# Optimization experiments

Hardware: AMD Instinct MI355X
Metric: run time of the kernel (lower is better)

The kernel has to match this reference:

```python
import jax, jax.numpy as jnp
import numpy as np

N = 50000      # num nodes
E = 800000     # num edges (before self loops)
DIN = 128      # input_dim
HID = 32       # hidden_dim per head
HEADS = 4
DOUT = 128     # output_dim
NEG_SLOPE = 0.2
EPS = 1e-5


def setup_inputs() -> dict:
    key = jax.random.key(0)
    ks = jax.random.split(key, 16)
    s = 0.05
    return {
        "x": jax.random.normal(ks[0], (N, DIN), dtype=jnp.float32),
        "edge_index": jax.random.randint(ks[1], (2, E), 0, N, dtype=jnp.int64),
        # GAT layer 1 (heads=4, concat=True)
        "W1": jax.random.normal(ks[2], (DIN, HEADS * HID), dtype=jnp.float32) * s,
        "att_src1": jax.random.normal(ks[3], (HEADS, HID), dtype=jnp.float32) * s,
        "att_dst1": jax.random.normal(ks[4], (HEADS, HID), dtype=jnp.float32) * s,
        "b1": jnp.zeros((HEADS * HID,), dtype=jnp.float32),
        # GAT layer 2 (heads=1, concat=False)
        "W2": jax.random.normal(ks[5], (HEADS * HID, DOUT), dtype=jnp.float32) * s,
        "att_src2": jax.random.normal(ks[6], (1, DOUT), dtype=jnp.float32) * s,
        "att_dst2": jax.random.normal(ks[7], (1, DOUT), dtype=jnp.float32) * s,
        "b2": jnp.zeros((DOUT,), dtype=jnp.float32),
        # LayerNorms
        "g1": jnp.ones((HEADS * HID,), dtype=jnp.float32),
        "be1": jnp.zeros((HEADS * HID,), dtype=jnp.float32),
        "g2": jnp.ones((DOUT,), dtype=jnp.float32),
        "be2": jnp.zeros((DOUT,), dtype=jnp.float32),
    }


def gat_conv(x, src, dst, W, a_src, a_dst, n_nodes):
    # x: [N, Fin]; W: [Fin, H*C]; a_src/a_dst: [H, C]
    H, C = a_src.shape
    h = (x @ W).reshape(-1, H, C)                       # [N, H, C]
    es = jnp.einsum("nhc,hc->nh", h, a_src)             # [N, H]
    ed = jnp.einsum("nhc,hc->nh", h, a_dst)             # [N, H]
    e = jax.nn.leaky_relu(es[src] + ed[dst], NEG_SLOPE)  # [E, H]
    # segment softmax over incoming edges of each dst node
    m = jax.ops.segment_max(e, dst, num_segments=n_nodes)
    a = jnp.exp(e - jax.lax.stop_gradient(m)[dst])
    den = jax.ops.segment_sum(a, dst, num_segments=n_nodes)
    alpha = a / den[dst]                                 # [E, H]
    out = jax.ops.segment_sum(alpha[:, :, None] * h[src], dst,
                              num_segments=n_nodes)      # [N, H, C]
    return out


def layer_norm(x, g, b):
    mu = jnp.mean(x, axis=-1, keepdims=True)
    var = jnp.mean((x - mu) ** 2, axis=-1, keepdims=True)
    return (x - mu) * jax.lax.rsqrt(var + EPS) * g + b


def reference(x, edge_index, W1, att_src1, att_dst1, b1,
              W2, att_src2, att_dst2, b2, g1, be1, g2, be2):
    n = x.shape[0]
    loop = jnp.arange(n, dtype=edge_index.dtype)
    src = jnp.concatenate([edge_index[0], loop])  # PyG add_self_loops=True
    dst = jnp.concatenate([edge_index[1], loop])

    h = gat_conv(x, src, dst, W1, att_src1, att_dst1, n)   # [N, 4, 32]
    h = h.reshape(n, -1) + b1                              # concat=True
    h = jax.nn.relu(layer_norm(h, g1, be1))                # dropout = id (eval)

    o = gat_conv(h, src, dst, W2, att_src2, att_dst2, n)   # [N, 1, DOUT]
    o = o[:, 0, :] + b2                                    # concat=False, 1 head
    o = jax.nn.relu(layer_norm(o, g2, be2))
    return o
```

## Files before the change

### kernel.cpp

```cpp
#include <hip/hip_runtime.h>

#define NEG 0.2f
#define LNEPS 1e-5f
#define BCAP 5120

static __device__ __forceinline__ float leaky(float e){ return fmaxf(e, NEG*e); }

static __device__ __forceinline__ unsigned pack_bf16(float a, float b){
  unsigned ua = __float_as_uint(a), ub = __float_as_uint(b);
  ua += 0x7FFFu + ((ua>>16)&1u);
  ub += 0x7FFFu + ((ub>>16)&1u);
  return (ua>>16) | (ub & 0xFFFF0000u);
}
static __device__ __forceinline__ float lo_bf(unsigned u){ return __uint_as_float(u<<16); }
static __device__ __forceinline__ float hi_bf(unsigned u){ return __uint_as_float(u & 0xFFFF0000u); }

typedef float f32x4 __attribute__((ext_vector_type(4)));
typedef short s16x8 __attribute__((ext_vector_type(8)));
union U4V8 { uint4 u; s16x8 v; };

static __device__ __forceinline__ void wave_scan256(int* sm, int t){
  if (t < 64){
    int a0=sm[t*4], a1=sm[t*4+1], a2=sm[t*4+2], a3=sm[t*4+3];
    int s = a0+a1+a2+a3, sc = s;
    #pragma unroll
    for (int o=1;o<64;o<<=1){ int x = __shfl_up(sc, o); if (t >= o) sc += x; }
    int e = sc - s;
    sm[t*4]   = e;
    sm[t*4+1] = e + a0;
    sm[t*4+2] = e + a0 + a1;
    sm[t*4+3] = e + a0 + a1 + a2;
  }
}


static __device__ __forceinline__ void wprep_body(int i, const float* __restrict__ W1,
                                                  const float* __restrict__ W2,
                                                  uint4* __restrict__ W1b, uint4* __restrict__ W2b){
  const float* W = (i < 2048) ? W1 : W2;
  uint4* Wb = (i < 2048) ? W1b : W2b;
  int ii = i & 2047;
  int lane = ii & 63, t = (ii>>6)&7, k0 = ii>>9;
  int c = lane & 15, q = lane >> 4;
  const float* base = &W[(size_t)(k0*32 + q*8)*128 + t*16 + c];
  uint4 u;
  u.x = pack_bf16(base[0*128], base[1*128]);
  u.y = pack_bf16(base[2*128], base[3*128]);
  u.z = pack_bf16(base[4*128], base[5*128]);
  u.w = pack_bf16(base[6*128], base[7*128]);
  Wb[ii] = u;
}

static __device__ void bstage_body(int bb, const int* __restrict__ src, const int* __restrict__ dst,
                                   int* __restrict__ bfill, unsigned* __restrict__ stage, int E){
  __shared__ int h[256];
  __shared__ int sm[256];
  __shared__ int sb[256];
  __shared__ int cur[256];
  __shared__ int rb[256];
  __shared__ unsigned buf[2048];
  int t = threadIdx.x;
  h[t] = 0; __syncthreads();
  int base = bb * 2048;
  int cnt = min(2048, E - base);
  for (int i = t; i < cnt; i += 256) atomicAdd(&h[((unsigned)dst[base+i]) >> 8], 1);
  __syncthreads();
  int hv = h[t];
  sm[t] = hv; __syncthreads();
  wave_scan256(sm, t);
  __syncthreads();
  int excl = sm[t];
  sb[t] = excl;
  cur[t] = excl;
  rb[t] = (hv > 0) ? atomicAdd(&bfill[t], hv) : 0;
  __syncthreads();
  for (int i = t; i < cnt; i += 256){
    unsigned d = (unsigned)dst[base+i];
    unsigned v = (unsigned)src[base+i] | (d << 16);
    int p = atomicAdd(&cur[d >> 8], 1);
    buf[p] = v;
  }
  __syncthreads();
  for (int i = t; i < cnt; i += 256){
    unsigned v = buf[i];
    int b = v >> 24;
    int slot = rb[b] + (i - sb[b]);
    if (slot < BCAP) stage[(size_t)b*BCAP + slot] = v;
  }
}

static __device__ void bucket_body(int b, const unsigned* __restrict__ stage, const int* __restrict__ bfill,
                                   int* __restrict__ offA, int* __restrict__ offB,
                                   unsigned* __restrict__ csr2, int N){
  __shared__ int cnt[256];
  __shared__ int sm[256];
  __shared__ int cur[256];
  int t = threadIdx.x;
  int lo = b * BCAP;
  int hi = lo + min(bfill[b], BCAP);
  cnt[t] = 0; __syncthreads();
  for (int i = lo + t; i < hi; i += 256) atomicAdd(&cnt[(stage[i] >> 16) & 0xFF], 1);
  __syncthreads();
  sm[t] = cnt[t]; __syncthreads();
  wave_scan256(sm, t);
  __syncthreads();
  int ex = sm[t];
  cur[t] = ex;
  int d = (b << 8) + t;
  if (d < N){ offA[d] = lo + ex; offB[d] = lo + ex + cnt[t]; }
  __syncthreads();
  for (int i = lo + t; i < hi; i += 256){
    unsigned v = stage[i];
    int p = atomicAdd(&cur[(v >> 16) & 0xFF], 1);
    csr2[(size_t)(lo + p)] = v;
  }
}

template<int HEADS, bool PACKED>
static __device__ void gemm_body(int bid, const float* __restrict__ A, const unsigned* __restrict__ Ab,
                                 const uint4* __restrict__ Wb,
                                 const float* __restrict__ as, const float* __restrict__ ad,
                                 unsigned* __restrict__ Hb, float* __restrict__ es,
                                 float* __restrict__ ed, float* __restrict__ m0, int n){
  __shared__ unsigned hstage[4][16*68];
  int tid = threadIdx.x;
  int wave = tid >> 6, lane = tid & 63;
  int c = lane & 15, q = lane >> 4;
  int r0 = bid*64 + wave*16;
  int rowa = r0 + c;
  int rowc = min(rowa, n-1);
  f32x4 acc[8];
  #pragma unroll
  for (int t=0;t<8;++t) acc[t] = (f32x4){0.f,0.f,0.f,0.f};

  #pragma unroll
  for (int k0 = 0; k0 < 4; ++k0){
    U4V8 af;
    if (PACKED){
      af.u = *(const uint4*)&Ab[(size_t)rowc*64 + k0*16 + q*4];
    } else {
      const float* ap = &A[(size_t)rowc*128 + k0*32 + q*8];
      float4 v0 = *(const float4*)ap;
      float4 v1 = *(const float4*)(ap+4);
      af.u.x = pack_bf16(v0.x, v0.y);
      af.u.y = pack_bf16(v0.z, v0.w);
      af.u.z = pack_bf16(v1.x, v1.y);
      af.u.w = pack_bf16(v1.z, v1.w);
    }
    #pragma unroll
    for (int t=0;t<8;++t){
      U4V8 bf;
      bf.u = Wb[(k0*8+t)*64 + lane];
      acc[t] = __builtin_amdgcn_mfma_f32_16x16x32_bf16(af.v, bf.v, acc[t], 0, 0, 0);
    }
  }

  float asv[8], adv[8];
  #pragma unroll
  for (int t=0;t<8;++t){ asv[t] = as[t*16+c]; adv[t] = ad[t*16+c]; }
  if (HEADS == 4){
    float pes[4][4], ped[4][4];
    #pragma unroll
    for (int r=0;r<4;++r)
      #pragma unroll
      for (int h=0;h<4;++h){ pes[r][h]=0.f; ped[r][h]=0.f; }
    #pragma unroll
    for (int t=0;t<8;++t)
      #pragma unroll
      for (int r=0;r<4;++r){
        pes[r][t>>1] = fmaf(acc[t][r], asv[t], pes[r][t>>1]);
        ped[r][t>>1] = fmaf(acc[t][r], adv[t], ped[r][t>>1]);
      }
    #pragma unroll
    for (int r=0;r<4;++r)
      #pragma unroll
      for (int h=0;h<4;++h){
        #pragma unroll
        for (int m=1;m<16;m<<=1){
          pes[r][h] += __shfl_xor(pes[r][h], m);
          ped[r][h] += __shfl_xor(ped[r][h], m);
        }
      }
    if (c == 0){
      #pragma unroll
      for (int r=0;r<4;++r){
        int row2 = r0 + q*4 + r;
        if (row2 < n){
          float4 e = make_float4(pes[r][0],pes[r][1],pes[r][2],pes[r][3]);
          float4 d = make_float4(ped[r][0],ped[r][1],ped[r][2],ped[r][3]);
          float4 mm = make_float4(leaky(e.x+d.x),leaky(e.y+d.y),leaky(e.z+d.z),leaky(e.w+d.w));
          *(float4*)&es[(size_t)row2*4] = e;
          *(float4*)&ed[(size_t)row2*4] = d;
          *(float4*)&m0[(size_t)row2*4] = mm;
        }
      }
    }
  } else {
    float pes[4] = {0.f,0.f,0.f,0.f}, ped[4] = {0.f,0.f,0.f,0.f};
    #pragma unroll
    for (int t=0;t<8;++t)
      #pragma unroll
      for (int r=0;r<4;++r){
        pes[r] = fmaf(acc[t][r], asv[t], pes[r]);
        ped[r] = fmaf(acc[t][r], adv[t], ped[r]);
      }
    #pragma unroll
    for (int r=0;r<4;++r){
      #pragma unroll
      for (int m=1;m<16;m<<=1){
        pes[r] += __shfl_xor(pes[r], m);
        ped[r] += __shfl_xor(ped[r], m);
      }
    }
    if (c == 0){
      #pragma unroll
      for (int r=0;r<4;++r){
        int row2 = r0 + q*4 + r;
        if (row2 < n){
          es[row2] = pes[r]; ed[row2] = ped[r]; m0[row2] = leaky(pes[r]+ped[r]);
        }
      }
    }
  }

  unsigned* hs = hstage[wave];
  #pragma unroll
  for (int t=0;t<8;++t)
    #pragma unroll
    for (int r=0;r<4;++r){
      float other = __shfl_xor(acc[t][r], 1);
      if (!(c & 1)) hs[(q*4+r)*68 + t*8 + (c>>1)] = pack_bf16(acc[t][r], other);
    }
  #pragma unroll
  for (int it=0; it<4; ++it){
    int idx = it*64 + lane;
    int rr = idx >> 4, c4 = idx & 15;
    int grow = r0 + rr;
    if (grow < n)
      *(uint4*)&Hb[(size_t)grow*64 + c4*4] = *(uint4*)&hs[rr*68 + c4*4];
  }
}


__global__ __launch_bounds__(256) void k_A(const float* __restrict__ W1, const float* __restrict__ W2,
                                           uint4* __restrict__ W1b, uint4* __restrict__ W2b,
                                           const int* __restrict__ src, const int* __restrict__ dst,
                                           int* __restrict__ bfill, unsigned* __restrict__ stage, int E){
  int bid = blockIdx.x;
  if (bid < 16){
    wprep_body(bid*256 + threadIdx.x, W1, W2, W1b, W2b);
  } else {
    bstage_body(bid - 16, src, dst, bfill, stage, E);
  }
}

__global__ __launch_bounds__(256) void k_B(const float* __restrict__ x, const uint4* __restrict__ W1b,
                                           const float* __restrict__ as1, const float* __restrict__ ad1,
                                           unsigned* __restrict__ Hb, float* __restrict__ es1,
                                           float* __restrict__ ed1, float* __restrict__ m01,
                                           const unsigned* __restrict__ stage, const int* __restrict__ bfill,
                                           int* __restrict__ offA, int* __restrict__ offB,
                                           unsigned* __restrict__ csr2, int N, int gb){
  int bid = blockIdx.x;
  if (bid < gb){
    gemm_body<4,false>(bid, x, nullptr, W1b, as1, ad1, Hb, es1, ed1, m01, N);
  } else {
    bucket_body(bid - gb, stage, bfill, offA, offB, csr2, N);
  }
}

template<int HEADS, bool PACKED>
__global__ __launch_bounds__(256) void k_gemm_mfma(const float* __restrict__ A,
                                                   const unsigned* __restrict__ Ab,
                                                   const uint4* __restrict__ Wb,
                                                   const float* __restrict__ as, const float* __restrict__ ad,
                                                   unsigned* __restrict__ Hb, float* __restrict__ es,
                                                   float* __restrict__ ed, float* __restrict__ m0, int n){
  gemm_body<HEADS,PACKED>(blockIdx.x, A, Ab, Wb, as, ad, Hb, es, ed, m0, n);
}


template<bool OUT_PACKED>
__global__ __launch_bounds__(256) void k_agg4(const unsigned* __restrict__ Hb,
                                              const float* __restrict__ es, const float* __restrict__ ed,
                                              const float* __restrict__ m0,
                                              const int* __restrict__ offA, const int* __restrict__ offB,
                                              const unsigned* __restrict__ csr2,
                                              const float* __restrict__ bias, const float* __restrict__ g,
                                              const float* __restrict__ be, float* __restrict__ out,
                                              unsigned* __restrict__ outp, int N){
  int lane = threadIdx.x & 63;
  int node = blockIdx.x*4 + (threadIdx.x >> 6);
  if (node >= N) return;
  int hh = lane >> 4;
  int wsrc = lane & 48;
  float edn = ed[(size_t)node*4 + hh];
  float m0n = m0[(size_t)node*4 + hh];
  float l = 1.f;
  unsigned uself = Hb[(size_t)node*64 + lane];
  float a1 = lo_bf(uself), a2 = hi_bf(uself);
  int j0 = offA[node], j1 = offB[node];
  for (int c0 = j0; c0 < j1; c0 += 16){
    int m = min(16, j1 - c0);
    int eidx = lane & 15;
    int sv = 0; float wv = 0.f;
    if (eidx < m){
      unsigned v = csr2[c0 + eidx];
      sv = v & 0xFFFF;
      wv = __expf(leaky(es[(size_t)sv*4 + hh] + edn) - m0n);
    }
    int j = 0;
    for (; j+7 < m; j += 8){
      int s0 = __shfl(sv, j),   s1 = __shfl(sv, j+1), s2 = __shfl(sv, j+2), s3 = __shfl(sv, j+3);
      int s4 = __shfl(sv, j+4), s5 = __shfl(sv, j+5), s6 = __shfl(sv, j+6), s7 = __shfl(sv, j+7);
      float w0 = __shfl(wv, wsrc | j),     w1 = __shfl(wv, wsrc | (j+1));
      float w2 = __shfl(wv, wsrc | (j+2)), w3 = __shfl(wv, wsrc | (j+3));
      float w4 = __shfl(wv, wsrc | (j+4)), w5 = __shfl(wv, wsrc | (j+5));
      float w6 = __shfl(wv, wsrc | (j+6)), w7 = __shfl(wv, wsrc | (j+7));
      unsigned u0 = Hb[(size_t)s0*64 + lane];
      unsigned u1 = Hb[(size_t)s1*64 + lane];
      unsigned u2 = Hb[(size_t)s2*64 + lane];
      unsigned u3 = Hb[(size_t)s3*64 + lane];
      unsigned u4 = Hb[(size_t)s4*64 + lane];
      unsigned u5 = Hb[(size_t)s5*64 + lane];
      unsigned u6 = Hb[(size_t)s6*64 + lane];
      unsigned u7 = Hb[(size_t)s7*64 + lane];
      l += ((w0 + w1) + (w2 + w3)) + ((w4 + w5) + (w6 + w7));
      a1 = fmaf(w0, lo_bf(u0), a1); a2 = fmaf(w0, hi_bf(u0), a2);
      a1 = fmaf(w1, lo_bf(u1), a1); a2 = fmaf(w1, hi_bf(u1), a2);
      a1 = fmaf(w2, lo_bf(u2), a1); a2 = fmaf(w2, hi_bf(u2), a2);
      a1 = fmaf(w3, lo_bf(u3), a1); a2 = fmaf(w3, hi_bf(u3), a2);
      a1 = fmaf(w4, lo_bf(u4), a1); a2 = fmaf(w4, hi_bf(u4), a2);
      a1 = fmaf(w5, lo_bf(u5), a1); a2 = fmaf(w5, hi_bf(u5), a2);
      a1 = fmaf(w6, lo_bf(u6), a1); a2 = fmaf(w6, hi_bf(u6), a2);
      a1 = fmaf(w7, lo_bf(u7), a1); a2 = fmaf(w7, hi_bf(u7), a2);
    }
    for (; j+3 < m; j += 4){
      int s0 = __shfl(sv, j), s1 = __shfl(sv, j+1), s2 = __shfl(sv, j+2), s3 = __shfl(sv, j+3);
      float w0 = __shfl(wv, wsrc | j),     w1 = __shfl(wv, wsrc | (j+1));
      float w2 = __shfl(wv, wsrc | (j+2)), w3 = __shfl(wv, wsrc | (j+3));
      unsigned u0 = Hb[(size_t)s0*64 + lane];
      unsigned u1 = Hb[(size_t)s1*64 + lane];
      unsigned u2 = Hb[(size_t)s2*64 + lane];
      unsigned u3 = Hb[(size_t)s3*64 + lane];
      l += (w0 + w1) + (w2 + w3);
      a1 = fmaf(w0, lo_bf(u0), a1); a2 = fmaf(w0, hi_bf(u0), a2);
      a1 = fmaf(w1, lo_bf(u1), a1); a2 = fmaf(w1, hi_bf(u1), a2);
      a1 = fmaf(w2, lo_bf(u2), a1); a2 = fmaf(w2, hi_bf(u2), a2);
      a1 = fmaf(w3, lo_bf(u3), a1); a2 = fmaf(w3, hi_bf(u3), a2);
    }
    for (; j < m; ++j){
      int s0 = __shfl(sv, j);
      float w0 = __shfl(wv, wsrc | j);
      unsigned u0 = Hb[(size_t)s0*64 + lane];
      l += w0;
      a1 = fmaf(w0, lo_bf(u0), a1); a2 = fmaf(w0, hi_bf(u0), a2);
    }
  }
  float rl = __frcp_rn(l);
  float2 bv = *(const float2*)&bias[2*lane];
  float v1 = a1 * rl + bv.x;
  float v2 = a2 * rl + bv.y;
  float s = v1 + v2;
  #pragma unroll
  for (int m=32;m>0;m>>=1) s += __shfl_xor(s,m);
  float mu = s * (1.f/128.f);
  float d1 = v1-mu, d2 = v2-mu;
  float ss = d1*d1 + d2*d2;
  #pragma unroll
  for (int m=32;m>0;m>>=1) ss += __shfl_xor(ss,m);
  float rs = rsqrtf(ss*(1.f/128.f) + LNEPS);
  float2 gv = *(const float2*)&g[2*lane];
  float2 bev = *(const float2*)&be[2*lane];
  float y1 = fmaxf(d1*rs*gv.x + bev.x, 0.f);
  float y2 = fmaxf(d2*rs*gv.y + bev.y, 0.f);
  if (OUT_PACKED){
    outp[(size_t)node*64 + lane] = pack_bf16(y1, y2);
  } else {
    *(float2*)&out[(size_t)node*128 + 2*lane] = make_float2(y1, y2);
  }
}

__global__ __launch_bounds__(256) void k_agg1(const unsigned* __restrict__ Hb,
                                              const float* __restrict__ es, const float* __restrict__ ed,
                                              const float* __restrict__ m0,
                                              const int* __restrict__ offA, const int* __restrict__ offB,
                                              const unsigned* __restrict__ csr2,
                                              const float* __restrict__ bias, const float* __restrict__ g,
                                              const float* __restrict__ be, float* __restrict__ out, int N){
  int lane = threadIdx.x & 63;
  int node = blockIdx.x*4 + (threadIdx.x >> 6);
  if (node >= N) return;
  float edn = ed[node];
  float m0n = m0[node];
  float l = 1.f;
  unsigned uself = Hb[(size_t)node*64 + lane];
  float a1 = lo_bf(uself), a2 = hi_bf(uself);
  int j0 = offA[node], j1 = offB[node];
  for (int c0 = j0; c0 < j1; c0 += 64){
    int m = min(64, j1 - c0);
    int sv = 0; float wv = 0.f;
    if (lane < m){
      unsigned v = csr2[c0 + lane];
      sv = v & 0xFFFF;
      wv = __expf(leaky(es[sv] + edn) - m0n);
    }
    int j = 0;
    for (; j+7 < m; j += 8){
      int s0 = __shfl(sv, j),   s1 = __shfl(sv, j+1), s2 = __shfl(sv, j+2), s3 = __shfl(sv, j+3);
      int s4 = __shfl(sv, j+4), s5 = __shfl(sv, j+5), s6 = __shfl(sv, j+6), s7 = __shfl(sv, j+7);
      float w0 = __shfl(wv, j),   w1 = __shfl(wv, j+1), w2 = __shfl(wv, j+2), w3 = __shfl(wv, j+3);
      float w4 = __shfl(wv, j+4), w5 = __shfl(wv, j+5), w6 = __shfl(wv, j+6), w7 = __shfl(wv, j+7);
      unsigned u0 = Hb[(size_t)s0*64 + lane];
      unsigned u1 = Hb[(size_t)s1*64 + lane];
      unsigned u2 = Hb[(size_t)s2*64 + lane];
      unsigned u3 = Hb[(size_t)s3*64 + lane];
      unsigned u4 = Hb[(size_t)s4*64 + lane];
      unsigned u5 = Hb[(size_t)s5*64 + lane];
      unsigned u6 = Hb[(size_t)s6*64 + lane];
      unsigned u7 = Hb[(size_t)s7*64 + lane];
      l += ((w0 + w1) + (w2 + w3)) + ((w4 + w5) + (w6 + w7));
      a1 = fmaf(w0, lo_bf(u0), a1); a2 = fmaf(w0, hi_bf(u0), a2);
      a1 = fmaf(w1, lo_bf(u1), a1); a2 = fmaf(w1, hi_bf(u1), a2);
      a1 = fmaf(w2, lo_bf(u2), a1); a2 = fmaf(w2, hi_bf(u2), a2);
      a1 = fmaf(w3, lo_bf(u3), a1); a2 = fmaf(w3, hi_bf(u3), a2);
      a1 = fmaf(w4, lo_bf(u4), a1); a2 = fmaf(w4, hi_bf(u4), a2);
      a1 = fmaf(w5, lo_bf(u5), a1); a2 = fmaf(w5, hi_bf(u5), a2);
      a1 = fmaf(w6, lo_bf(u6), a1); a2 = fmaf(w6, hi_bf(u6), a2);
      a1 = fmaf(w7, lo_bf(u7), a1); a2 = fmaf(w7, hi_bf(u7), a2);
    }
    for (; j+3 < m; j += 4){
      int s0 = __shfl(sv, j), s1 = __shfl(sv, j+1), s2 = __shfl(sv, j+2), s3 = __shfl(sv, j+3);
      float w0 = __shfl(wv, j), w1 = __shfl(wv, j+1), w2 = __shfl(wv, j+2), w3 = __shfl(wv, j+3);
      unsigned u0 = Hb[(size_t)s0*64 + lane];
      unsigned u1 = Hb[(size_t)s1*64 + lane];
      unsigned u2 = Hb[(size_t)s2*64 + lane];
      unsigned u3 = Hb[(size_t)s3*64 + lane];
      l += (w0 + w1) + (w2 + w3);
      a1 = fmaf(w0, lo_bf(u0), a1); a2 = fmaf(w0, hi_bf(u0), a2);
      a1 = fmaf(w1, lo_bf(u1), a1); a2 = fmaf(w1, hi_bf(u1), a2);
      a1 = fmaf(w2, lo_bf(u2), a1); a2 = fmaf(w2, hi_bf(u2), a2);
      a1 = fmaf(w3, lo_bf(u3), a1); a2 = fmaf(w3, hi_bf(u3), a2);
    }
    for (; j < m; ++j){
      int s0 = __shfl(sv, j);
      float w0 = __shfl(wv, j);
      unsigned u0 = Hb[(size_t)s0*64 + lane];
      l += w0;
      a1 = fmaf(w0, lo_bf(u0), a1); a2 = fmaf(w0, hi_bf(u0), a2);
    }
  }
  float rl = __frcp_rn(l);
  float2 bv = *(const float2*)&bias[2*lane];
  float v1 = a1 * rl + bv.x;
  float v2 = a2 * rl + bv.y;
  float s = v1 + v2;
  #pragma unroll
  for (int mm=32;mm>0;mm>>=1) s += __shfl_xor(s,mm);
  float mu = s * (1.f/128.f);
  float d1 = v1-mu, d2 = v2-mu;
  float ss = d1*d1 + d2*d2;
  #pragma unroll
  for (int mm=32;mm>0;mm>>=1) ss += __shfl_xor(ss,mm);
  float rs = rsqrtf(ss*(1.f/128.f) + LNEPS);
  float2 gv = *(const float2*)&g[2*lane];
  float2 bev = *(const float2*)&be[2*lane];
  float y1 = fmaxf(d1*rs*gv.x + bev.x, 0.f);
  float y2 = fmaxf(d2*rs*gv.y + bev.y, 0.f);
  *(float2*)&out[(size_t)node*128 + 2*lane] = make_float2(y1, y2);
}


extern "C" void kernel_launch(void* const* d_in, const int* in_sizes, int n_in,
                              void* d_out, int out_size, void* d_ws, size_t ws_size,
                              hipStream_t stream){
  const float* x   = (const float*)d_in[0];
  const int*   ei  = (const int*)  d_in[1];
  const float* W1  = (const float*)d_in[2];
  const float* as1 = (const float*)d_in[3];
  const float* ad1 = (const float*)d_in[4];
  const float* b1  = (const float*)d_in[5];
  const float* W2  = (const float*)d_in[6];
  const float* as2 = (const float*)d_in[7];
  const float* ad2 = (const float*)d_in[8];
  const float* b2  = (const float*)d_in[9];
  const float* g1  = (const float*)d_in[10];
  const float* be1 = (const float*)d_in[11];
  const float* g2  = (const float*)d_in[12];
  const float* be2 = (const float*)d_in[13];

  int N = in_sizes[0] / 128;
  int E = in_sizes[1] / 2;
  const int* src = ei;
  const int* dst = ei + E;

  int NB = (N + 255) >> 8;

  char* p = (char*)d_ws;
  auto carve = [&](size_t bytes)->char*{ char* r = p; p += ((bytes + 255) / 256) * 256; return r; };
  unsigned* Hb = (unsigned*)carve((size_t)N*64*4);
  unsigned* Bb = (unsigned*)carve((size_t)N*64*4);
  float* es1 = (float*)carve((size_t)N*4*4);
  float* ed1 = (float*)carve((size_t)N*4*4);
  float* m01 = (float*)carve((size_t)N*4*4);
  float* es2 = (float*)carve((size_t)N*4);
  float* ed2 = (float*)carve((size_t)N*4);
  float* m02 = (float*)carve((size_t)N*4);
  int* offA  = (int*)carve((size_t)N*4);
  int* offB  = (int*)carve((size_t)N*4);
  unsigned* stg  = (unsigned*)carve((size_t)NB*BCAP*4);
  unsigned* csr2 = (unsigned*)carve((size_t)NB*BCAP*4);
  uint4* W1b = (uint4*)carve(2048*16);
  uint4* W2b = (uint4*)carve(2048*16);
  int* bfill = (int*)carve(256*4);

  hipMemsetAsync(bfill, 0, 1024, stream);

  int nbe = (E + 2047) / 2048;
  int gb  = (N + 63) / 64;
  int nb4 = (N + 3) / 4;

  k_A<<<16 + nbe, 256, 0, stream>>>(W1, W2, W1b, W2b, src, dst, bfill, stg, E);
  k_B<<<gb + NB, 256, 0, stream>>>(x, W1b, as1, ad1, Hb, es1, ed1, m01,
                                   stg, bfill, offA, offB, csr2, N, gb);
  k_agg4<true><<<nb4, 256, 0, stream>>>(Hb, es1, ed1, m01, offA, offB, csr2,
                                        b1, g1, be1, nullptr, Bb, N);
  k_gemm_mfma<1,true><<<gb, 256, 0, stream>>>(nullptr, Bb, W2b, as2, ad2, Hb, es2, ed2, m02, N);
  k_agg1<<<nb4, 256, 0, stream>>>(Hb, es2, ed2, m02, offA, offB, csr2,
                                  b2, g2, be2, (float*)d_out, N);
}
```

Before: 226.1 us.

## Split waves into edge-parallel lane groups with 128-bit bf16 feature gathers

The agg4 and agg1 aggregation kernels are restructured so each wave runs as four 16-lane groups. Each group handles a different neighbor edge, and each lane gathers 8 bf16 features with a single uint4 load instead of one 32-bit load per lane per edge. Partial sums are combined across groups with xor shuffles, and the self-loop term is added afterwards. LayerNorm then runs on 8 values per lane over 16 lanes, with only group 0 writing output. The aim is fewer, wider gather instructions and more memory requests in flight per edge. The cost is more registers, a cross-group reduction, and wasted work on padded edges in partial chunks.

Result: no change. 223.5 us (-1.2%).

```diff
diff --git a/kernel.cpp b/kernel.cpp
--- a/kernel.cpp
+++ b/kernel.cpp
@@ -18,6 +18,17 @@
 typedef float f32x4 __attribute__((ext_vector_type(4)));
 typedef short s16x8 __attribute__((ext_vector_type(8)));
 union U4V8 { uint4 u; s16x8 v; };
+
+static __device__ __forceinline__ void acc8(float w, uint4 u, float* a){
+  a[0] = fmaf(w, lo_bf(u.x), a[0]);
+  a[1] = fmaf(w, hi_bf(u.x), a[1]);
+  a[2] = fmaf(w, lo_bf(u.y), a[2]);
+  a[3] = fmaf(w, hi_bf(u.y), a[3]);
+  a[4] = fmaf(w, lo_bf(u.z), a[4]);
+  a[5] = fmaf(w, hi_bf(u.z), a[5]);
+  a[6] = fmaf(w, lo_bf(u.w), a[6]);
+  a[7] = fmaf(w, hi_bf(u.w), a[7]);
+}
 
 static __device__ __forceinline__ void wave_scan256(int* sm, int t){
   if (t < 64){
@@ -292,92 +303,95 @@
   int lane = threadIdx.x & 63;
   int node = blockIdx.x*4 + (threadIdx.x >> 6);
   if (node >= N) return;
-  int hh = lane >> 4;
-  int wsrc = lane & 48;
-  float edn = ed[(size_t)node*4 + hh];
-  float m0n = m0[(size_t)node*4 + hh];
-  float l = 1.f;
-  unsigned uself = Hb[(size_t)node*64 + lane];
-  float a1 = lo_bf(uself), a2 = hi_bf(uself);
+  int grp = lane >> 4;
+  int fi  = lane & 15;
+  int hsrc = (fi >> 2) << 4;
+  float edn = ed[(size_t)node*4 + grp];
+  float m0n = m0[(size_t)node*4 + grp];
+  float a[8];
+  #pragma unroll
+  for (int k=0;k<8;++k) a[k] = 0.f;
+  float l = 0.f;
   int j0 = offA[node], j1 = offB[node];
   for (int c0 = j0; c0 < j1; c0 += 16){
-    int m = min(16, j1 - c0);
-    int eidx = lane & 15;
+    int m = j1 - c0;
     int sv = 0; float wv = 0.f;
-    if (eidx < m){
-      unsigned v = csr2[c0 + eidx];
+    if (fi < m){
+      unsigned v = csr2[c0 + fi];
       sv = v & 0xFFFF;
-      wv = __expf(leaky(es[(size_t)sv*4 + hh] + edn) - m0n);
-    }
-    int j = 0;
-    for (; j+7 < m; j += 8){
-      int s0 = __shfl(sv, j),   s1 = __shfl(sv, j+1), s2 = __shfl(sv, j+2), s3 = __shfl(sv, j+3);
-      int s4 = __shfl(sv, j+4), s5 = __shfl(sv, j+5), s6 = __shfl(sv, j+6), s7 = __shfl(sv, j+7);
-      float w0 = __shfl(wv, wsrc | j),     w1 = __shfl(wv, wsrc | (j+1));
-      float w2 = __shfl(wv, wsrc | (j+2)), w3 = __shfl(wv, wsrc | (j+3));
-      float w4 = __shfl(wv, wsrc | (j+4)), w5 = __shfl(wv, wsrc | (j+5));
-      float w6 = __shfl(wv, wsrc | (j+6)), w7 = __shfl(wv, wsrc | (j+7));
-      unsigned u0 = Hb[(size_t)s0*64 + lane];
-      unsigned u1 = Hb[(size_t)s1*64 + lane];
-      unsigned u2 = Hb[(size_t)s2*64 + lane];
-      unsigned u3 = Hb[(size_t)s3*64 + lane];
-      unsigned u4 = Hb[(size_t)s4*64 + lane];
-      unsigned u5 = Hb[(size_t)s5*64 + lane];
-      unsigned u6 = Hb[(size_t)s6*64 + lane];
-      unsigned u7 = Hb[(size_t)s7*64 + lane];
-      l += ((w0 + w1) + (w2 + w3)) + ((w4 + w5) + (w6 + w7));
-      a1 = fmaf(w0, lo_bf(u0), a1); a2 = fmaf(w0, hi_bf(u0), a2);
-      a1 = fmaf(w1, lo_bf(u1), a1); a2 = fmaf(w1, hi_bf(u1), a2);
-      a1 = fmaf(w2, lo_bf(u2), a1); a2 = fmaf(w2, hi_bf(u2), a2);
-      a1 = fmaf(w3, lo_bf(u3), a1); a2 = fmaf(w3, hi_bf(u3), a2);
-      a1 = fmaf(w4, lo_bf(u4), a1); a2 = fmaf(w4, hi_bf(u4), a2);
-      a1 = fmaf(w5, lo_bf(u5), a1); a2 = fmaf(w5, hi_bf(u5), a2);
-      a1 = fmaf(w6, lo_bf(u6), a1); a2 = fmaf(w6, hi_bf(u6), a2);
-      a1 = fmaf(w7, lo_bf(u7), a1); a2 = fmaf(w7, hi_bf(u7), a2);
-    }
-    for (; j+3 < m; j += 4){
-      int s0 = __shfl(sv, j), s1 = __shfl(sv, j+1), s2 = __shfl(sv, j+2), s3 = __shfl(sv, j+3);
-      float w0 = __shfl(wv, wsrc | j),     w1 = __shfl(wv, wsrc | (j+1));
-      float w2 = __shfl(wv, wsrc | (j+2)), w3 = __shfl(wv, wsrc | (j+3));
-      unsigned u0 = Hb[(size_t)s0*64 + lane];
-      unsigned u1 = Hb[(size_t)s1*64 + lane];
-      unsigned u2 = Hb[(size_t)s2*64 + lane];
-      unsigned u3 = Hb[(size_t)s3*64 + lane];
-      l += (w0 + w1) + (w2 + w3);
-      a1 = fmaf(w0, lo_bf(u0), a1); a2 = fmaf(w0, hi_bf(u0), a2);
-      a1 = fmaf(w1, lo_bf(u1), a1); a2 = fmaf(w1, hi_bf(u1), a2);
-      a1 = fmaf(w2, lo_bf(u2), a1); a2 = fmaf(w2, hi_bf(u2), a2);
-      a1 = fmaf(w3, lo_bf(u3), a1); a2 = fmaf(w3, hi_bf(u3), a2);
-    }
-    for (; j < m; ++j){
-      int s0 = __shfl(sv, j);
-      float w0 = __shfl(wv, wsrc | j);
-      unsigned u0 = Hb[(size_t)s0*64 + lane];
-      l += w0;
-      a1 = fmaf(w0, lo_bf(u0), a1); a2 = fmaf(w0, hi_bf(u0), a2);
-    }
-  }
+      wv = __expf(leaky(es[(size_t)sv*4 + grp] + edn) - m0n);
+    }
+    int   s0 = __shfl(sv, grp),          s1 = __shfl(sv, 4 + grp),
+          s2 = __shfl(sv, 8 + grp),      s3 = __shfl(sv, 12 + grp);
+    float w0 = __shfl(wv, hsrc + grp),   w1 = __shfl(wv, hsrc + 4 + grp),
+          w2 = __shfl(wv, hsrc + 8 + grp), w3 = __shfl(wv, hsrc + 12 + grp);
+    uint4 u0 = *(const uint4*)&Hb[(size_t)s0*64 + fi*4];
+    uint4 u1 = *(const uint4*)&Hb[(size_t)s1*64 + fi*4];
+    uint4 u2 = *(const uint4*)&Hb[(size_t)s2*64 + fi*4];
+    uint4 u3 = *(const uint4*)&Hb[(size_t)s3*64 + fi*4];
+    l += ((w0 + w1) + (w2 + w3));
+    acc8(w0, u0, a);
+    acc8(w1, u1, a);
+    acc8(w2, u2, a);
+    acc8(w3, u3, a);
+  }
+  #pragma unroll
+  for (int k=0;k<8;++k){
+    a[k] += __shfl_xor(a[k], 16);
+    a[k] += __shfl_xor(a[k], 32);
+  }
+  l += __shfl_xor(l, 16);
+  l += __shfl_xor(l, 32);
+  uint4 us = *(const uint4*)&Hb[(size_t)node*64 + fi*4];
+  a[0] += lo_bf(us.x); a[1] += hi_bf(us.x);
+  a[2] += lo_bf(us.y); a[3] += hi_bf(us.y);
+  a[4] += lo_bf(us.z); a[5] += hi_bf(us.z);
+  a[6] += lo_bf(us.w); a[7] += hi_bf(us.w);
+  l += 1.f;
+
   float rl = __frcp_rn(l);
-  float2 bv = *(const float2*)&bias[2*lane];
-  float v1 = a1 * rl + bv.x;
-  float v2 = a2 * rl + bv.y;
-  float s = v1 + v2;
-  #pragma unroll
-  for (int m=32;m>0;m>>=1) s += __shfl_xor(s,m);
+  float4 bv0 = *(const float4*)&bias[fi*8];
+  float4 bv1 = *(const float4*)&bias[fi*8 + 4];
+  float v[8];
+  v[0] = a[0]*rl + bv0.x; v[1] = a[1]*rl + bv0.y;
+  v[2] = a[2]*rl + bv0.z; v[3] = a[3]*rl + bv0.w;
+  v[4] = a[4]*rl + bv1.x; v[5] = a[5]*rl + bv1.y;
+  v[6] = a[6]*rl + bv1.z; v[7] = a[7]*rl + bv1.w;
+  float s = ((v[0]+v[1])+(v[2]+v[3])) + ((v[4]+v[5])+(v[6]+v[7]));
+  #pragma unroll
+  for (int mm=1; mm<16; mm<<=1) s += __shfl_xor(s, mm);
   float mu = s * (1.f/128.f);
-  float d1 = v1-mu, d2 = v2-mu;
-  float ss = d1*d1 + d2*d2;
-  #pragma unroll
-  for (int m=32;m>0;m>>=1) ss += __shfl_xor(ss,m);
+  float d[8], ss = 0.f;
+  #pragma unroll
+  for (int k=0;k<8;++k){ d[k] = v[k]-mu; ss += d[k]*d[k]; }
+  #pragma unroll
+  for (int mm=1; mm<16; mm<<=1) ss += __shfl_xor(ss, mm);
   float rs = rsqrtf(ss*(1.f/128.f) + LNEPS);
-  float2 gv = *(const float2*)&g[2*lane];
-  float2 bev = *(const float2*)&be[2*lane];
-  float y1 = fmaxf(d1*rs*gv.x + bev.x, 0.f);
-  float y2 = fmaxf(d2*rs*gv.y + bev.y, 0.f);
-  if (OUT_PACKED){
-    outp[(size_t)node*64 + lane] = pack_bf16(y1, y2);
-  } else {
-    *(float2*)&out[(size_t)node*128 + 2*lane] = make_float2(y1, y2);
+  float4 gv0 = *(const float4*)&g[fi*8];
+  float4 gv1 = *(const float4*)&g[fi*8 + 4];
+  float4 ev0 = *(const float4*)&be[fi*8];
+  float4 ev1 = *(const float4*)&be[fi*8 + 4];
+  float y[8];
+  y[0] = fmaxf(d[0]*rs*gv0.x + ev0.x, 0.f);
+  y[1] = fmaxf(d[1]*rs*gv0.y + ev0.y, 0.f);
+  y[2] = fmaxf(d[2]*rs*gv0.z + ev0.z, 0.f);
+  y[3] = fmaxf(d[3]*rs*gv0.w + ev0.w, 0.f);
+  y[4] = fmaxf(d[4]*rs*gv1.x + ev1.x, 0.f);
+  y[5] = fmaxf(d[5]*rs*gv1.y + ev1.y, 0.f);
+  y[6] = fmaxf(d[6]*rs*gv1.z + ev1.z, 0.f);
+  y[7] = fmaxf(d[7]*rs*gv1.w + ev1.w, 0.f);
+  if (grp == 0){
+    if (OUT_PACKED){
+      uint4 o;
+      o.x = pack_bf16(y[0], y[1]);
+      o.y = pack_bf16(y[2], y[3]);
+      o.z = pack_bf16(y[4], y[5]);
+      o.w = pack_bf16(y[6], y[7]);
+      *(uint4*)&outp[(size_t)node*64 + fi*4] = o;
+    } else {
+      *(float4*)&out[(size_t)node*128 + fi*8]     = make_float4(y[0],y[1],y[2],y[3]);
+      *(float4*)&out[(size_t)node*128 + fi*8 + 4] = make_float4(y[4],y[5],y[6],y[7]);
+    }
   }
 }
 
@@ -391,11 +405,14 @@
   int lane = threadIdx.x & 63;
   int node = blockIdx.x*4 + (threadIdx.x >> 6);
   if (node >= N) return;
+  int grp = lane >> 4;
+  int fi  = lane & 15;
   float edn = ed[node];
   float m0n = m0[node];
-  float l = 1.f;
-  unsigned uself = Hb[(size_t)node*64 + lane];
-  float a1 = lo_bf(uself), a2 = hi_bf(uself);
+  float a[8];
+  #pragma unroll
+  for (int k=0;k<8;++k) a[k] = 0.f;
+  float l = 0.f;
   int j0 = offA[node], j1 = offB[node];
   for (int c0 = j0; c0 < j1; c0 += 64){
     int m = min(64, j1 - c0);
@@ -405,69 +422,71 @@
       sv = v & 0xFFFF;
       wv = __expf(leaky(es[sv] + edn) - m0n);
     }
-    int j = 0;
-    for (; j+7 < m; j += 8){
-      int s0 = __shfl(sv, j),   s1 = __shfl(sv, j+1), s2 = __shfl(sv, j+2), s3 = __shfl(sv, j+3);
-      int s4 = __shfl(sv, j+4), s5 = __shfl(sv, j+5), s6 = __shfl(sv, j+6), s7 = __shfl(sv, j+7);
-      float w0 = __shfl(wv, j),   w1 = __shfl(wv, j+1), w2 = __shfl(wv, j+2), w3 = __shfl(wv, j+3);
-      float w4 = __shfl(wv, j+4), w5 = __shfl(wv, j+5), w6 = __shfl(wv, j+6), w7 = __shfl(wv, j+7);
-      unsigned u0 = Hb[(size_t)s0*64 + lane];
-      unsigned u1 = Hb[(size_t)s1*64 + lane];
-      unsigned u2 = Hb[(size_t)s2*64 + lane];
-      unsigned u3 = Hb[(size_t)s3*64 + lane];
-      unsigned u4 = Hb[(size_t)s4*64 + lane];
-      unsigned u5 = Hb[(size_t)s5*64 + lane];
-      unsigned u6 = Hb[(size_t)s6*64 + lane];
-      unsigned u7 = Hb[(size_t)s7*64 + lane];
-      l += ((w0 + w1) + (w2 + w3)) + ((w4 + w5) + (w6 + w7));
-      a1 = fmaf(w0, lo_bf(u0), a1); a2 = fmaf(w0, hi_bf(u0), a2);
-      a1 = fmaf(w1, lo_bf(u1), a1); a2 = fmaf(w1, hi_bf(u1), a2);
-      a1 = fmaf(w2, lo_bf(u2), a1); a2 = fmaf(w2, hi_bf(u2), a2);
-      a1 = fmaf(w3, lo_bf(u3), a1); a2 = fmaf(w3, hi_bf(u3), a2);
-      a1 = fmaf(w4, lo_bf(u4), a1); a2 = fmaf(w4, hi_bf(u4), a2);
-      a1 = fmaf(w5, lo_bf(u5), a1); a2 = fmaf(w5, hi_bf(u5), a2);
-      a1 = fmaf(w6, lo_bf(u6), a1); a2 = fmaf(w6, hi_bf(u6), a2);
-      a1 = fmaf(w7, lo_bf(u7), a1); a2 = fmaf(w7, hi_bf(u7), a2);
-    }
-    for (; j+3 < m; j += 4){
-      int s0 = __shfl(sv, j), s1 = __shfl(sv, j+1), s2 = __shfl(sv, j+2), s3 = __shfl(sv, j+3);
-      float w0 = __shfl(wv, j), w1 = __shfl(wv, j+1), w2 = __shfl(wv, j+2), w3 = __shfl(wv, j+3);
-      unsigned u0 = Hb[(size_t)s0*64 + lane];
-      unsigned u1 = Hb[(size_t)s1*64 + lane];
-      unsigned u2 = Hb[(size_t)s2*64 + lane];
-      unsigned u3 = Hb[(size_t)s3*64 + lane];
-      l += (w0 + w1) + (w2 + w3);
-      a1 = fmaf(w0, lo_bf(u0), a1); a2 = fmaf(w0, hi_bf(u0), a2);
-      a1 = fmaf(w1, lo_bf(u1), a1); a2 = fmaf(w1, hi_bf(u1), a2);
-      a1 = fmaf(w2, lo_bf(u2), a1); a2 = fmaf(w2, hi_bf(u2), a2);
-      a1 = fmaf(w3, lo_bf(u3), a1); a2 = fmaf(w3, hi_bf(u3), a2);
-    }
-    for (; j < m; ++j){
-      int s0 = __shfl(sv, j);
-      float w0 = __shfl(wv, j);
-      unsigned u0 = Hb[(size_t)s0*64 + lane];
-      l += w0;
-      a1 = fmaf(w0, lo_bf(u0), a1); a2 = fmaf(w0, hi_bf(u0), a2);
-    }
-  }
+    for (int jj = 0; jj < m; jj += 16){
+      int   s0 = __shfl(sv, jj + grp),      s1 = __shfl(sv, jj + 4 + grp),
+            s2 = __shfl(sv, jj + 8 + grp),  s3 = __shfl(sv, jj + 12 + grp);
+      float w0 = __shfl(wv, jj + grp),      w1 = __shfl(wv, jj + 4 + grp),
+            w2 = __shfl(wv, jj + 8 + grp),  w3 = __shfl(wv, jj + 12 + grp);
+      uint4 u0 = *(const uint4*)&Hb[(size_t)s0*64 + fi*4];
+      uint4 u1 = *(const uint4*)&Hb[(size_t)s1*64 + fi*4];
+      uint4 u2 = *(const uint4*)&Hb[(size_t)s2*64 + fi*4];
+      uint4 u3 = *(const uint4*)&Hb[(size_t)s3*64 + fi*4];
+      l += ((w0 + w1) + (w2 + w3));
+      acc8(w0, u0, a);
+      acc8(w1, u1, a);
+      acc8(w2, u2, a);
+      acc8(w3, u3, a);
+    }
+  }
+  #pragma unroll
+  for (int k=0;k<8;++k){
+    a[k] += __shfl_xor(a[k], 16);
+    a[k] += __shfl_xor(a[k], 32);
+  }
+  l += __shfl_xor(l, 16);
+  l += __shfl_xor(l, 32);
+  uint4 us = *(const uint4*)&Hb[(size_t)node*64 + fi*4];
+  a[0] += lo_bf(us.x); a[1] += hi_bf(us.x);
+  a[2] += lo_bf(us.y); a[3] += hi_bf(us.y);
+  a[4] += lo_bf(us.z); a[5] += hi_bf(us.z);
+  a[6] += lo_bf(us.w); a[7] += hi_bf(us.w);
+  l += 1.f;
+
   float rl = __frcp_rn(l);
-  float2 bv = *(const float2*)&bias[2*lane];
-  float v1 = a1 * rl + bv.x;
-  float v2 = a2 * rl + bv.y;
-  float s = v1 + v2;
-  #pragma unroll
-  for (int mm=32;mm>0;mm>>=1) s += __shfl_xor(s,mm);
+  float4 bv0 = *(const float4*)&bias[fi*8];
+  float4 bv1 = *(const float4*)&bias[fi*8 + 4];
+  float v[8];
+  v[0] = a[0]*rl + bv0.x; v[1] = a[1]*rl + bv0.y;
+  v[2] = a[2]*rl + bv0.z; v[3] = a[3]*rl + bv0.w;
+  v[4] = a[4]*rl + bv1.x; v[5] = a[5]*rl + bv1.y;
+  v[6] = a[6]*rl + bv1.z; v[7] = a[7]*rl + bv1.w;
+  float s = ((v[0]+v[1])+(v[2]+v[3])) + ((v[4]+v[5])+(v[6]+v[7]));
+  #pragma unroll
+  for (int mm=1; mm<16; mm<<=1) s += __shfl_xor(s, mm);
   float mu = s * (1.f/128.f);
-  float d1 = v1-mu, d2 = v2-mu;
-  float ss = d1*d1 + d2*d2;
-  #pragma unroll
-  for (int mm=32;mm>0;mm>>=1) ss += __shfl_xor(ss,mm);
+  float d[8], ss = 0.f;
+  #pragma unroll
+  for (int k=0;k<8;++k){ d[k] = v[k]-mu; ss += d[k]*d[k]; }
+  #pragma unroll
+  for (int mm=1; mm<16; mm<<=1) ss += __shfl_xor(ss, mm);
   float rs = rsqrtf(ss*(1.f/128.f) + LNEPS);
-  float2 gv = *(const float2*)&g[2*lane];
-  float2 bev = *(const float2*)&be[2*lane];
-  float y1 = fmaxf(d1*rs*gv.x + bev.x, 0.f);
-  float y2 = fmaxf(d2*rs*gv.y + bev.y, 0.f);
-  *(float2*)&out[(size_t)node*128 + 2*lane] = make_float2(y1, y2);
+  float4 gv0 = *(const float4*)&g[fi*8];
+  float4 gv1 = *(const float4*)&g[fi*8 + 4];
+  float4 ev0 = *(const float4*)&be[fi*8];
+  float4 ev1 = *(const float4*)&be[fi*8 + 4];
+  float y[8];
+  y[0] = fmaxf(d[0]*rs*gv0.x + ev0.x, 0.f);
+  y[1] = fmaxf(d[1]*rs*gv0.y + ev0.y, 0.f);
+  y[2] = fmaxf(d[2]*rs*gv0.z + ev0.z, 0.f);
+  y[3] = fmaxf(d[3]*rs*gv0.w + ev0.w, 0.f);
+  y[4] = fmaxf(d[4]*rs*gv1.x + ev1.x, 0.f);
+  y[5] = fmaxf(d[5]*rs*gv1.y + ev1.y, 0.f);
+  y[6] = fmaxf(d[6]*rs*gv1.z + ev1.z, 0.f);
+  y[7] = fmaxf(d[7]*rs*gv1.w + ev1.w, 0.f);
+  if (grp == 0){
+    *(float4*)&out[(size_t)node*128 + fi*8]     = make_float4(y[0],y[1],y[2],y[3]);
+    *(float4*)&out[(size_t)node*128 + fi*8 + 4] = make_float4(y[4],y[5],y[6],y[7]);
+  }
 }
 
 
```
